# Optimization experiments

Measured on AMD Instinct MI355X. Metric: run time of the kernel, lower is better.

The kernel has to match this reference:

```python
import jax, jax.numpy as jnp
import numpy as np

IOU_THRESHOLD = 0.5
CLASS_CONF_THRESHOLD = 0.01
MAX_OUTPUT = 100  # tf.image.non_max_suppression max_output_size


def _nms_indices(boxes, scores, max_out, iou_thr):
    """Fixed-size greedy NMS: returns (idxs[max_out], valid[max_out])."""
    x1, y1, x2, y2 = boxes[:, 0], boxes[:, 1], boxes[:, 2], boxes[:, 3]
    areas = (x2 - x1) * (y2 - y1)

    def body(sc, _):
        i = jnp.argmax(sc)
        valid = sc[i] > 0.0  # score_threshold = 0.0 in tf call
        xx1 = jnp.maximum(x1[i], x1)
        yy1 = jnp.maximum(y1[i], y1)
        xx2 = jnp.minimum(x2[i], x2)
        yy2 = jnp.minimum(y2[i], y2)
        inter = jnp.maximum(xx2 - xx1, 0.0) * jnp.maximum(yy2 - yy1, 0.0)
        union = areas[i] + areas - inter
        iou = jnp.where(union > 0.0, inter / union, 0.0)
        # suppress overlapping boxes (self included, iou=1) only if pick valid
        sc_new = jnp.where((iou > iou_thr) & valid, -1.0, sc)
        return sc_new, (i, valid)

    _, (idxs, valids) = jax.lax.scan(body, scores, None, length=max_out)
    return idxs, valids


def _decode(x, anchors):
    B, H, W, A, C = x.shape  # B == 1
    gw = jnp.float32(W)
    # grid offsets: (col, row) per cell, matching cell_x / transposed cell_y
    cx = jnp.broadcast_to(jnp.arange(W, dtype=jnp.float32).reshape(1, 1, W, 1, 1), (1, H, W, 1, 1))
    cy = jnp.broadcast_to(jnp.arange(H, dtype=jnp.float32).reshape(1, H, 1, 1, 1), (1, H, W, 1, 1))
    grid = jnp.concatenate([cx, cy], axis=-1)  # (1,H,W,1,2)

    xy = (jax.nn.sigmoid(x[..., 0:2]) + grid) / gw                      # (B,H,W,A,2)
    wh = jnp.exp(x[..., 2:4]) * anchors.reshape(1, 1, 1, A, 2) / gw     # (B,H,W,A,2)
    boxes = jnp.concatenate([xy - wh / 2.0, xy + wh / 2.0], axis=-1)    # (B,H,W,A,4)

    conf = jax.nn.sigmoid(x[..., 4:5])                                  # (B,H,W,A,1)
    cls_prob = jax.nn.softmax(x[..., 5:], axis=-1)                      # (B,H,W,A,C-5)
    class_confidence = conf * cls_prob
    masked = jnp.where(class_confidence > CLASS_CONF_THRESHOLD, class_confidence, 0.0)
    classes = jnp.argmax(masked, axis=-1).astype(jnp.int32)             # (B,H,W,A)
    confm = jnp.max(masked, axis=-1)                                    # (B,H,W,A)

    N = H * W * A
    return boxes.reshape(N, 4), confm.reshape(N), classes.reshape(N)


def reference(x, anchors):
    boxes, scores, classes = _decode(x, anchors)
    idxs, valids = _nms_indices(jax.lax.stop_gradient(boxes),
                                jax.lax.stop_gradient(scores),
                                MAX_OUTPUT, IOU_THRESHOLD)
    sel_conf = jnp.where(valids, scores[idxs], 0.0)
    sel_boxes = jnp.where(valids[:, None], boxes[idxs], 0.0)
    sel_classes = jnp.where(valids, classes[idxs], -1)
    return sel_conf, sel_boxes, sel_classes


def setup_inputs() -> dict:
    key = jax.random.key(0)
    k1, k2 = jax.random.split(key)
    x = jax.random.normal(k1, (1, 256, 256, 5, 85), dtype=jnp.float32)
    # anchor priors in grid units (positive widths/heights)
    anchors = jax.random.uniform(k2, (5, 2), dtype=jnp.float32) * 4.0 + 0.5
    return {"x": x, "anchors": anchors}
```

## Files before the change

### kernel.cpp

```cpp
#include <hip/hip_runtime.h>
#include <hip/hip_bf16.h>

#define NROW 327680
#define NCLS 80
#define K_TARGET 1024u
#define CAP 2048u
#define MAX_OUT 100
#define NBIN 864
#define BIN0 0x3C23
#define HIST_BLOCKS 80

#define WS_BOXES    0
#define WS_SCORES   5242880
#define WS_CLASSES  6553600
#define WS_HIST     7864320

typedef __attribute__((address_space(1))) const unsigned int g_uint;
typedef __attribute__((address_space(3))) unsigned int lds_uint;

__device__ __forceinline__ void async_copy16(const float* g, float* l) {
  __builtin_amdgcn_global_load_lds((const g_uint*)g, (lds_uint*)l, 16, 0, 0);
}

__global__ __launch_bounds__(64) void decode_kernel(
    const float* __restrict__ x, const float* __restrict__ anchors,
    float4* __restrict__ boxes, float* __restrict__ scores,
    int* __restrict__ classes) {
  __shared__ float lds[64 * 85];
  const int t = threadIdx.x;
  const int row0 = blockIdx.x * 64;
  const float* gbase = x + (size_t)row0 * 85;

  #pragma unroll
  for (int i = 0; i < 21; ++i) {
    const int idx = i * 64 + t;
    async_copy16(gbase + idx * 4, lds + idx * 4);
  }
  if (t < 16) {
    const int idx = 1344 + t;
    async_copy16(gbase + idx * 4, lds + idx * 4);
  }
  __syncthreads();

  const float* row = lds + t * 85;
  const int r = row0 + t;

  float m = row[5]; int am = 0;
  for (int c = 1; c < NCLS; ++c) { float l = row[5 + c]; if (l > m) { m = l; am = c; } }
  float s = 0.f;
  for (int c = 0; c < NCLS; ++c) s += expf(row[5 + c] - m);
  float conf = 1.f / (1.f + expf(-row[4]));
  float p = 1.f / s;
  float best = conf * p;
  float score; int cls;
  if (best > 0.01f) { score = best; cls = am; } else { score = 0.f; cls = 0; }

  const int a  = r % 5;
  const int hw = r / 5;
  const float wf = (float)(hw & 255);
  const float hf = (float)(hw >> 8);
  float sx = 1.f / (1.f + expf(-row[0]));
  float sy = 1.f / (1.f + expf(-row[1]));
  float xc = (sx + wf) / 256.f;
  float yc = (sy + hf) / 256.f;
  float bw = expf(row[2]) * anchors[2*a]     / 256.f;
  float bh = expf(row[3]) * anchors[2*a + 1] / 256.f;
  float hwd = bw / 2.f, hhd = bh / 2.f;

  boxes[r]   = make_float4(xc - hwd, yc - hhd, xc + hwd, yc + hhd);
  scores[r]  = score;
  classes[r] = cls;
}

__global__ __launch_bounds__(1024) void hist_kernel(
    const float* __restrict__ scores, unsigned* __restrict__ part) {
  __shared__ unsigned h[NBIN];
  const int t = threadIdx.x;
  if (t < NBIN) h[t] = 0;
  __syncthreads();

  float4 s4 = ((const float4*)scores)[blockIdx.x * 1024 + t];
  float sv[4] = {s4.x, s4.y, s4.z, s4.w};
  #pragma unroll
  for (int k = 0; k < 4; ++k) {
    float s = sv[k];
    if (s > 0.f) {
      int idx = (int)(__float_as_uint(s) >> 16) - BIN0;
      if (idx > NBIN - 1) idx = NBIN - 1;
      atomicAdd(&h[idx], 1u);
    }
  }
  __syncthreads();
  if (t < NBIN) part[blockIdx.x * NBIN + t] = h[t];
}

__global__ __launch_bounds__(1024) void nms_fused(
    const float* __restrict__ scores, const float4* __restrict__ boxes,
    const int* __restrict__ classes, const unsigned* __restrict__ part,
    float* __restrict__ out) {
  __shared__ unsigned bufA[1024], bufB[1024];
  __shared__ unsigned Tsh, ncand;
  __shared__ unsigned long long sk[CAP];
  __shared__ float4 cbox[CAP];
  __shared__ float4 kbox[MAX_OUT];
  __shared__ float  kscore[MAX_OUT];
  __shared__ int    krow[MAX_OUT];
  __shared__ int    knum;
  const int t = threadIdx.x;
  if (t == 0) { ncand = 0; knum = 0; }

  unsigned colsum = 0;
  if (t < NBIN) {
    unsigned a0 = 0, a1 = 0, a2 = 0, a3 = 0;
    #pragma unroll
    for (int b = 0; b < HIST_BLOCKS; b += 4) {
      a0 += part[(b + 0) * NBIN + t];
      a1 += part[(b + 1) * NBIN + t];
      a2 += part[(b + 2) * NBIN + t];
      a3 += part[(b + 3) * NBIN + t];
    }
    colsum = a0 + a1 + a2 + a3;
  }
  bufA[t] = colsum;
  __syncthreads();

  unsigned* src = bufA; unsigned* dst = bufB;
  for (int d = 1; d < 1024; d <<= 1) {
    unsigned val = src[t] + ((t + d < 1024) ? src[t + d] : 0u);
    dst[t] = val;
    __syncthreads();
    unsigned* tmp = src; src = dst; dst = tmp;
  }
  if (src[t] >= K_TARGET && (t == 1023 || src[t + 1] < K_TARGET)) {
    unsigned T = (unsigned)t;
    if (src[t] > CAP) T += 1;
    Tsh = T;
  }
  if (t == 0 && src[0] < K_TARGET) Tsh = 0;
  __syncthreads();
  const unsigned T = Tsh;

  const float4* s4p = (const float4*)scores;
  for (int j = 0; j < 80; j += 4) {
    float4 q[4];
    q[0] = s4p[(j + 0) * 1024 + t];
    q[1] = s4p[(j + 1) * 1024 + t];
    q[2] = s4p[(j + 2) * 1024 + t];
    q[3] = s4p[(j + 3) * 1024 + t];
    #pragma unroll
    for (int u = 0; u < 4; ++u) {
      float sv[4] = {q[u].x, q[u].y, q[u].z, q[u].w};
      #pragma unroll
      for (int k = 0; k < 4; ++k) {
        float s = sv[k];
        if (s <= 0.f) continue;
        unsigned bits = __float_as_uint(s);
        int idx = (int)(bits >> 16) - BIN0;
        if (idx > NBIN - 1) idx = NBIN - 1;
        if ((unsigned)idx < T) continue;
        unsigned pos = atomicAdd(&ncand, 1u);
        unsigned r = (unsigned)(((j + u) * 1024 + t) * 4 + k);
        if (pos < CAP)
          sk[pos] = ((unsigned long long)bits << 32) |
                    (unsigned long long)(0xFFFFFFFFu - r);
      }
    }
  }
  __syncthreads();
  unsigned n = ncand; if (n > CAP) n = CAP;
  unsigned npow2 = 2; while (npow2 < n) npow2 <<= 1;
  for (unsigned i = t; i < npow2; i += 1024) if (i >= n) sk[i] = 0ull;
  __syncthreads();

  for (unsigned k = 2; k <= npow2; k <<= 1) {
    for (unsigned j = k >> 1; j > 0; j >>= 1) {
      for (unsigned i = t; i < npow2; i += 1024) {
        unsigned ixj = i ^ j;
        if (ixj > i) {
          unsigned long long a = sk[i], b = sk[ixj];
          bool desc = ((i & k) == 0);
          if (desc ? (a < b) : (a > b)) { sk[i] = b; sk[ixj] = a; }
        }
      }
      __syncthreads();
    }
  }

  for (unsigned i = t; i < n; i += 1024) {
    unsigned r = 0xFFFFFFFFu - (unsigned)(sk[i] & 0xFFFFFFFFull);
    cbox[i] = boxes[r];
  }
  __syncthreads();

  if (t < 64) {
    int nk = 0;
    float ax1=0,ay1=0,ax2=0,ay2=0,aar=0;
    float bx1=0,by1=0,bx2=0,by2=0,bar=0;
    for (unsigned cc = 0; cc < n && nk < MAX_OUT; ++cc) {
      unsigned long long key = sk[cc];
      unsigned sbits = (unsigned)(key >> 32);
      if (sbits == 0u) break;
      float4 bb = cbox[cc];
      float area = (bb.z - bb.x) * (bb.w - bb.y);
      bool s0 = false, s1 = false;
      if (t < nk) {
        float xx1 = fmaxf(ax1, bb.x), yy1 = fmaxf(ay1, bb.y);
        float xx2 = fminf(ax2, bb.z), yy2 = fminf(ay2, bb.w);
        float inter = fmaxf(xx2 - xx1, 0.f) * fmaxf(yy2 - yy1, 0.f);
        float uni = aar + area - inter;
        s0 = (uni > 0.f) && (inter / uni > 0.5f);
      }
      if (t + 64 < nk) {
        float xx1 = fmaxf(bx1, bb.x), yy1 = fmaxf(by1, bb.y);
        float xx2 = fminf(bx2, bb.z), yy2 = fminf(by2, bb.w);
        float inter = fmaxf(xx2 - xx1, 0.f) * fmaxf(yy2 - yy1, 0.f);
        float uni = bar + area - inter;
        s1 = (uni > 0.f) && (inter / uni > 0.5f);
      }
      if (!__any(s0 || s1)) {
        if (t == nk)      { ax1=bb.x; ay1=bb.y; ax2=bb.z; ay2=bb.w; aar=area; }
        if (t == nk - 64) { bx1=bb.x; by1=bb.y; bx2=bb.z; by2=bb.w; bar=area; }
        if (t == 0) {
          unsigned r = 0xFFFFFFFFu - (unsigned)(key & 0xFFFFFFFFull);
          kbox[nk] = bb; kscore[nk] = __uint_as_float(sbits); krow[nk] = (int)r;
        }
        ++nk;
      }
    }
    if (t == 0) knum = nk;
  }
  __syncthreads();

  if (t < MAX_OUT) {
    float confv = 0.f; float4 bb = make_float4(0.f, 0.f, 0.f, 0.f); float cf = -1.f;
    if (t < knum) { confv = kscore[t]; bb = kbox[t]; cf = (float)classes[krow[t]]; }
    out[t] = confv;
    ((float4*)(out + 100))[t] = bb;
    out[500 + t] = cf;
  }
}

extern "C" void kernel_launch(void* const* d_in, const int* in_sizes, int n_in,
                              void* d_out, int out_size, void* d_ws, size_t ws_size,
                              hipStream_t stream) {
  const float* x       = (const float*)d_in[0];
  const float* anchors = (const float*)d_in[1];
  float* out = (float*)d_out;
  char* ws = (char*)d_ws;

  float4*   boxes   = (float4*)(ws + WS_BOXES);
  float*    scores  = (float*)(ws + WS_SCORES);
  int*      classes = (int*)(ws + WS_CLASSES);
  unsigned* part    = (unsigned*)(ws + WS_HIST);

  hipLaunchKernelGGL(decode_kernel, dim3(NROW / 64), dim3(64),
                     0, stream, x, anchors, boxes, scores, classes);
  hipLaunchKernelGGL(hist_kernel, dim3(HIST_BLOCKS), dim3(1024),
                     0, stream, scores, part);
  hipLaunchKernelGGL(nms_fused, dim3(1), dim3(1024), 0, stream,
                     scores, boxes, classes, part, out);
}
```

Baseline: 268.2 us.

## Decode boxes/classes lazily for candidates and parallelize candidate compaction across blocks

```diff
diff --git a/kernel.cpp b/kernel.cpp
--- a/kernel.cpp
+++ b/kernel.cpp
@@ -8,12 +8,11 @@
 #define MAX_OUT 100
 #define NBIN 864
 #define BIN0 0x3C23
-#define HIST_BLOCKS 80
-
-#define WS_BOXES    0
-#define WS_SCORES   5242880
-#define WS_CLASSES  6553600
-#define WS_HIST     7864320
+
+#define WS_SCORES 0
+#define WS_HIST   1310720
+#define WS_CNT    1314176
+#define WS_KEYS   1314240
 
 typedef __attribute__((address_space(1))) const unsigned int g_uint;
 typedef __attribute__((address_space(3))) unsigned int lds_uint;
@@ -22,10 +21,8 @@
   __builtin_amdgcn_global_load_lds((const g_uint*)g, (lds_uint*)l, 16, 0, 0);
 }
 
-__global__ __launch_bounds__(64) void decode_kernel(
-    const float* __restrict__ x, const float* __restrict__ anchors,
-    float4* __restrict__ boxes, float* __restrict__ scores,
-    int* __restrict__ classes) {
+__global__ __launch_bounds__(64) void decode_score(
+    const float* __restrict__ x, float* __restrict__ scores) {
   __shared__ float lds[64 * 85];
   const int t = threadIdx.x;
   const int row0 = blockIdx.x * 64;
@@ -43,37 +40,18 @@
   __syncthreads();
 
   const float* row = lds + t * 85;
-  const int r = row0 + t;
-
-  float m = row[5]; int am = 0;
-  for (int c = 1; c < NCLS; ++c) { float l = row[5 + c]; if (l > m) { m = l; am = c; } }
+  float m = row[5];
+  for (int c = 1; c < NCLS; ++c) { float l = row[5 + c]; if (l > m) m = l; }
   float s = 0.f;
   for (int c = 0; c < NCLS; ++c) s += expf(row[5 + c] - m);
   float conf = 1.f / (1.f + expf(-row[4]));
   float p = 1.f / s;
   float best = conf * p;
-  float score; int cls;
-  if (best > 0.01f) { score = best; cls = am; } else { score = 0.f; cls = 0; }
-
-  const int a  = r % 5;
-  const int hw = r / 5;
-  const float wf = (float)(hw & 255);
-  const float hf = (float)(hw >> 8);
-  float sx = 1.f / (1.f + expf(-row[0]));
-  float sy = 1.f / (1.f + expf(-row[1]));
-  float xc = (sx + wf) / 256.f;
-  float yc = (sy + hf) / 256.f;
-  float bw = expf(row[2]) * anchors[2*a]     / 256.f;
-  float bh = expf(row[3]) * anchors[2*a + 1] / 256.f;
-  float hwd = bw / 2.f, hhd = bh / 2.f;
-
-  boxes[r]   = make_float4(xc - hwd, yc - hhd, xc + hwd, yc + hhd);
-  scores[r]  = score;
-  classes[r] = cls;
+  scores[row0 + t] = (best > 0.01f) ? best : 0.f;
 }
 
 __global__ __launch_bounds__(1024) void hist_kernel(
-    const float* __restrict__ scores, unsigned* __restrict__ part) {
+    const float* __restrict__ scores, unsigned* __restrict__ hist) {
   __shared__ unsigned h[NBIN];
   const int t = threadIdx.x;
   if (t < NBIN) h[t] = 0;
@@ -91,15 +69,70 @@
     }
   }
   __syncthreads();
-  if (t < NBIN) part[blockIdx.x * NBIN + t] = h[t];
-}
-
-__global__ __launch_bounds__(1024) void nms_fused(
-    const float* __restrict__ scores, const float4* __restrict__ boxes,
-    const int* __restrict__ classes, const unsigned* __restrict__ part,
+  if (t < NBIN && h[t]) atomicAdd(&hist[t], h[t]);
+}
+
+__global__ __launch_bounds__(1024) void thresh_kernel(
+    const unsigned* __restrict__ hist, unsigned* __restrict__ cnt) {
+  __shared__ unsigned bufA[1024], bufB[1024];
+  const int t = threadIdx.x;
+  bufA[t] = (t < NBIN) ? hist[t] : 0u;
+  __syncthreads();
+  unsigned* src = bufA; unsigned* dst = bufB;
+  for (int d = 1; d < 1024; d <<= 1) {
+    unsigned val = src[t] + ((t + d < 1024) ? src[t + d] : 0u);
+    dst[t] = val;
+    __syncthreads();
+    unsigned* tmp = src; src = dst; dst = tmp;
+  }
+  if (src[t] >= K_TARGET && (t == 1023 || src[t + 1] < K_TARGET)) {
+    unsigned T = (unsigned)t;
+    if (src[t] > CAP) T += 1;
+    cnt[1] = T;
+  }
+  if (t == 0 && src[0] < K_TARGET) cnt[1] = 0;
+}
+
+__global__ __launch_bounds__(256) void compact_kernel(
+    const float* __restrict__ scores, unsigned* __restrict__ cnt,
+    unsigned long long* __restrict__ keys) {
+  __shared__ unsigned blocal, bbase;
+  const int t = threadIdx.x;
+  if (t == 0) blocal = 0;
+  __syncthreads();
+
+  const unsigned T = cnt[1];
+  const int gi = blockIdx.x * 256 + t;
+  float4 s4 = ((const float4*)scores)[gi];
+  float sv[4] = {s4.x, s4.y, s4.z, s4.w};
+  unsigned long long lk[4]; int nl = 0;
+  #pragma unroll
+  for (int k = 0; k < 4; ++k) {
+    float s = sv[k];
+    if (s <= 0.f) continue;
+    unsigned bits = __float_as_uint(s);
+    int idx = (int)(bits >> 16) - BIN0;
+    if (idx > NBIN - 1) idx = NBIN - 1;
+    if ((unsigned)idx < T) continue;
+    unsigned r = (unsigned)(gi * 4 + k);
+    lk[nl++] = ((unsigned long long)bits << 32) |
+               (unsigned long long)(0xFFFFFFFFu - r);
+  }
+  unsigned lpos = nl ? atomicAdd(&blocal, (unsigned)nl) : 0u;
+  __syncthreads();
+  if (t == 0 && blocal) bbase = atomicAdd(&cnt[0], blocal);
+  __syncthreads();
+  if (nl) {
+    unsigned base = bbase + lpos;
+    for (int i = 0; i < nl; ++i)
+      if (base + i < CAP) keys[base + i] = lk[i];
+  }
+}
+
+__global__ __launch_bounds__(1024) void final_kernel(
+    const float* __restrict__ x, const float* __restrict__ anchors,
+    const unsigned* __restrict__ cnt, const unsigned long long* __restrict__ keys,
     float* __restrict__ out) {
-  __shared__ unsigned bufA[1024], bufB[1024];
-  __shared__ unsigned Tsh, ncand;
   __shared__ unsigned long long sk[CAP];
   __shared__ float4 cbox[CAP];
   __shared__ float4 kbox[MAX_OUT];
@@ -107,69 +140,11 @@
   __shared__ int    krow[MAX_OUT];
   __shared__ int    knum;
   const int t = threadIdx.x;
-  if (t == 0) { ncand = 0; knum = 0; }
-
-  unsigned colsum = 0;
-  if (t < NBIN) {
-    unsigned a0 = 0, a1 = 0, a2 = 0, a3 = 0;
-    #pragma unroll
-    for (int b = 0; b < HIST_BLOCKS; b += 4) {
-      a0 += part[(b + 0) * NBIN + t];
-      a1 += part[(b + 1) * NBIN + t];
-      a2 += part[(b + 2) * NBIN + t];
-      a3 += part[(b + 3) * NBIN + t];
-    }
-    colsum = a0 + a1 + a2 + a3;
-  }
-  bufA[t] = colsum;
-  __syncthreads();
-
-  unsigned* src = bufA; unsigned* dst = bufB;
-  for (int d = 1; d < 1024; d <<= 1) {
-    unsigned val = src[t] + ((t + d < 1024) ? src[t + d] : 0u);
-    dst[t] = val;
-    __syncthreads();
-    unsigned* tmp = src; src = dst; dst = tmp;
-  }
-  if (src[t] >= K_TARGET && (t == 1023 || src[t + 1] < K_TARGET)) {
-    unsigned T = (unsigned)t;
-    if (src[t] > CAP) T += 1;
-    Tsh = T;
-  }
-  if (t == 0 && src[0] < K_TARGET) Tsh = 0;
-  __syncthreads();
-  const unsigned T = Tsh;
-
-  const float4* s4p = (const float4*)scores;
-  for (int j = 0; j < 80; j += 4) {
-    float4 q[4];
-    q[0] = s4p[(j + 0) * 1024 + t];
-    q[1] = s4p[(j + 1) * 1024 + t];
-    q[2] = s4p[(j + 2) * 1024 + t];
-    q[3] = s4p[(j + 3) * 1024 + t];
-    #pragma unroll
-    for (int u = 0; u < 4; ++u) {
-      float sv[4] = {q[u].x, q[u].y, q[u].z, q[u].w};
-      #pragma unroll
-      for (int k = 0; k < 4; ++k) {
-        float s = sv[k];
-        if (s <= 0.f) continue;
-        unsigned bits = __float_as_uint(s);
-        int idx = (int)(bits >> 16) - BIN0;
-        if (idx > NBIN - 1) idx = NBIN - 1;
-        if ((unsigned)idx < T) continue;
-        unsigned pos = atomicAdd(&ncand, 1u);
-        unsigned r = (unsigned)(((j + u) * 1024 + t) * 4 + k);
-        if (pos < CAP)
-          sk[pos] = ((unsigned long long)bits << 32) |
-                    (unsigned long long)(0xFFFFFFFFu - r);
-      }
-    }
-  }
-  __syncthreads();
-  unsigned n = ncand; if (n > CAP) n = CAP;
+  if (t == 0) knum = 0;
+
+  unsigned n = cnt[0]; if (n > CAP) n = CAP;
   unsigned npow2 = 2; while (npow2 < n) npow2 <<= 1;
-  for (unsigned i = t; i < npow2; i += 1024) if (i >= n) sk[i] = 0ull;
+  for (unsigned i = t; i < npow2; i += 1024) sk[i] = (i < n) ? keys[i] : 0ull;
   __syncthreads();
 
   for (unsigned k = 2; k <= npow2; k <<= 1) {
@@ -188,7 +163,20 @@
 
   for (unsigned i = t; i < n; i += 1024) {
     unsigned r = 0xFFFFFFFFu - (unsigned)(sk[i] & 0xFFFFFFFFull);
-    cbox[i] = boxes[r];
+    const float* rp = x + (size_t)r * 85;
+    float tx = rp[0], ty = rp[1], tw = rp[2], th = rp[3];
+    const int a  = (int)(r % 5u);
+    const int hw = (int)(r / 5u);
+    const float wf = (float)(hw & 255);
+    const float hf = (float)(hw >> 8);
+    float sx = 1.f / (1.f + expf(-tx));
+    float sy = 1.f / (1.f + expf(-ty));
+    float xc = (sx + wf) / 256.f;
+    float yc = (sy + hf) / 256.f;
+    float bw = expf(tw) * anchors[2*a]     / 256.f;
+    float bh = expf(th) * anchors[2*a + 1] / 256.f;
+    float hwd = bw / 2.f, hhd = bh / 2.f;
+    cbox[i] = make_float4(xc - hwd, yc - hhd, xc + hwd, yc + hhd);
   }
   __syncthreads();
 
@@ -232,9 +220,15 @@
   __syncthreads();
 
   if (t < MAX_OUT) {
-    float confv = 0.f; float4 bb = make_float4(0.f, 0.f, 0.f, 0.f); float cf = -1.f;
-    if (t < knum) { confv = kscore[t]; bb = kbox[t]; cf = (float)classes[krow[t]]; }
-    out[t] = confv;
+    float conf = 0.f; float4 bb = make_float4(0.f, 0.f, 0.f, 0.f); float cf = -1.f;
+    if (t < knum) {
+      conf = kscore[t]; bb = kbox[t];
+      const float* rp = x + (size_t)krow[t] * 85;
+      float m = rp[5]; int am = 0;
+      for (int c = 1; c < NCLS; ++c) { float l = rp[5 + c]; if (l > m) { m = l; am = c; } }
+      cf = (float)am;
+    }
+    out[t] = conf;
     ((float4*)(out + 100))[t] = bb;
     out[500 + t] = cf;
   }
@@ -248,15 +242,20 @@
   float* out = (float*)d_out;
   char* ws = (char*)d_ws;
 
-  float4*   boxes   = (float4*)(ws + WS_BOXES);
-  float*    scores  = (float*)(ws + WS_SCORES);
-  int*      classes = (int*)(ws + WS_CLASSES);
-  unsigned* part    = (unsigned*)(ws + WS_HIST);
-
-  hipLaunchKernelGGL(decode_kernel, dim3(NROW / 64), dim3(64),
-                     0, stream, x, anchors, boxes, scores, classes);
-  hipLaunchKernelGGL(hist_kernel, dim3(HIST_BLOCKS), dim3(1024),
-                     0, stream, scores, part);
-  hipLaunchKernelGGL(nms_fused, dim3(1), dim3(1024), 0, stream,
-                     scores, boxes, classes, part, out);
-}
+  float*              scores = (float*)(ws + WS_SCORES);
+  unsigned*           hist   = (unsigned*)(ws + WS_HIST);
+  unsigned*           cnt    = (unsigned*)(ws + WS_CNT);
+  unsigned long long* keys   = (unsigned long long*)(ws + WS_KEYS);
+
+  hipMemsetAsync(hist, 0, NBIN * sizeof(unsigned) + 64, stream);
+
+  hipLaunchKernelGGL(decode_score, dim3(NROW / 64), dim3(64),
+                     0, stream, x, scores);
+  hipLaunchKernelGGL(hist_kernel, dim3(NROW / 4096), dim3(1024),
+                     0, stream, scores, hist);
+  hipLaunchKernelGGL(thresh_kernel, dim3(1), dim3(1024), 0, stream, hist, cnt);
+  hipLaunchKernelGGL(compact_kernel, dim3(NROW / 1024), dim3(256),
+                     0, stream, scores, cnt, keys);
+  hipLaunchKernelGGL(final_kernel, dim3(1), dim3(1024), 0, stream,
+                     x, anchors, cnt, keys, out);
+}
```

After: 249.3 us. 1.08x faster.
